# Kernel optimization log

Hardware: AMD Instinct MI355X
Metric: run time of the kernel (lower is better)

## Reference

```python
import jax, jax.numpy as jnp
import numpy as np

N_NODES = 50000
N_EDGES = 800000
N_GRAPHS = 100
IN_DIM = 100
OUT_DIM = 128
N_ETYPES = 4
N_STEPS = 8


def setup_inputs() -> dict:
    key = jax.random.key(0)
    ks = jax.random.split(key, 16)
    s = 0.05
    return {
        "features": jax.random.normal(ks[0], (N_NODES, IN_DIM), jnp.float32),
        "edge_src": jax.random.randint(ks[1], (N_EDGES,), 0, N_NODES, jnp.int32),
        "edge_dst": jax.random.randint(ks[2], (N_EDGES,), 0, N_NODES, jnp.int32),
        "edge_types": jax.random.randint(ks[3], (N_EDGES,), 0, N_ETYPES, jnp.int32),
        "graph_ids": jnp.sort(jax.random.randint(ks[4], (N_NODES,), 0, N_GRAPHS, jnp.int32)),
        "W_msg": jax.random.normal(ks[5], (N_ETYPES, OUT_DIM, OUT_DIM), jnp.float32) * s,
        "b_msg": jax.random.normal(ks[6], (N_ETYPES, OUT_DIM), jnp.float32) * s,
        "W_ih": jax.random.normal(ks[7], (3 * OUT_DIM, OUT_DIM), jnp.float32) * s,
        "W_hh": jax.random.normal(ks[8], (3 * OUT_DIM, OUT_DIM), jnp.float32) * s,
        "b_ih": jax.random.normal(ks[9], (3 * OUT_DIM,), jnp.float32) * s,
        "b_hh": jax.random.normal(ks[10], (3 * OUT_DIM,), jnp.float32) * s,
        "W1": jax.random.normal(ks[11], (256, OUT_DIM), jnp.float32) * s,
        "b1": jax.random.normal(ks[12], (256,), jnp.float32) * s,
        "W2": jax.random.normal(ks[13], (1, 256), jnp.float32) * s,
        "b2": jax.random.normal(ks[14], (1,), jnp.float32) * s,
    }


def _gru_cell(x, h, W_ih, W_hh, b_ih, b_hh):
    # torch.nn.GRUCell: gate order (reset, update, new)
    gi = x @ W_ih.T + b_ih  # [N, 3D]
    gh = h @ W_hh.T + b_hh
    i_r, i_z, i_n = jnp.split(gi, 3, axis=-1)
    h_r, h_z, h_n = jnp.split(gh, 3, axis=-1)
    r = jax.nn.sigmoid(i_r + h_r)
    z = jax.nn.sigmoid(i_z + h_z)
    n = jnp.tanh(i_n + r * h_n)
    return (1.0 - z) * n + z * h


def reference(features, edge_src, edge_dst, edge_types, graph_ids,
              W_msg, b_msg, W_ih, W_hh, b_ih, b_hh, W1, b1, W2, b2):
    n_nodes = features.shape[0]
    # DGL GatedGraphConv: zero-pad input features to out_feats
    h = jnp.pad(features, ((0, 0), (0, OUT_DIM - features.shape[1])))
    for _ in range(N_STEPS):
        # per-edge-type linear transform of source features: [T, N, D]
        transformed = jnp.einsum('nd,tdf->tnf', h, W_msg) + b_msg[:, None, :]
        msgs = transformed[edge_types, edge_src]  # [E, D] gather
        a = jax.ops.segment_sum(msgs, edge_dst, num_segments=n_nodes)  # scatter-add
        h = _gru_cell(a, h, W_ih, W_hh, b_ih, b_hh)
    # masked mean pooling per graph (mask_mean over de-batchified graphs)
    counts = jax.ops.segment_sum(jnp.ones((n_nodes,), h.dtype), graph_ids,
                                 num_segments=N_GRAPHS)
    sums = jax.ops.segment_sum(h, graph_ids, num_segments=N_GRAPHS)
    pooled = sums / jnp.maximum(counts, 1.0)[:, None]  # [B, D]
    # classifier: Linear -> relu -> (dropout: eval noop) -> Linear -> sigmoid
    hidden = jax.nn.relu(pooled @ W1.T + b1)
    logits = hidden @ W2.T + b2  # [B, 1]
    return jax.nn.sigmoid(logits).squeeze(-1)  # [B]
```

## Files before the change

kernel.cpp:

```cpp
#include <hip/hip_runtime.h>
#include <hip/hip_bf16.h>
#include <math.h>

#define N_NODES 50000
#define M_PAD   50048
#define N_EDGES 800000
#define N_GRAPHS 100
#define IN_DIM 100
#define D 128
#define N_STEPS 8
#define NBINS (N_NODES * 4)
#define SCAN_BLOCKS 196

typedef unsigned short ushort_t;
typedef __bf16 bf16x8 __attribute__((ext_vector_type(8)));
typedef float f32x4 __attribute__((ext_vector_type(4)));

__device__ inline ushort_t f2b(float f) {
  __hip_bfloat16 b = __float2bfloat16(f);
  return *reinterpret_cast<ushort_t*>(&b);
}
__device__ inline float b2f(unsigned int u16) {
  unsigned int x = u16 << 16;
  return __builtin_bit_cast(float, x);
}

__device__ __attribute__((always_inline)) inline void gld16(const ushort_t* g, ushort_t* l) {
  __builtin_amdgcn_global_load_lds(
      (const __attribute__((address_space(1))) void*)g,
      (__attribute__((address_space(3))) void*)l, 16, 0, 0);
}

__global__ void pad_cast_kernel(const float* __restrict__ feat, ushort_t* __restrict__ h) {
  int idx = blockIdx.x * blockDim.x + threadIdx.x;
  if (idx >= N_NODES * D) return;
  int n = idx >> 7, d = idx & 127;
  float v = (d < IN_DIM) ? feat[n * IN_DIM + d] : 0.0f;
  h[(size_t)n * 128 + d] = f2b(v);
}

__global__ void prep_bts(const float* __restrict__ W_msg, ushort_t* __restrict__ BtS) {
  int idx = blockIdx.x * blockDim.x + threadIdx.x;
  if (idx >= 128 * 512) return;
  int f = idx >> 9, kp = idx & 511;
  int t = kp >> 7, k = kp & 127;
  BtS[(size_t)f * 512 + kp] = f2b(W_msg[((size_t)t * 128 + k) * 128 + f]);
}

__global__ void prep_wg(const float* __restrict__ W_ih, const float* __restrict__ W_hh,
                        const float* __restrict__ b_ih, const float* __restrict__ b_hh,
                        ushort_t* __restrict__ WgT, float* __restrict__ gbias) {
  int idx = blockIdx.x * blockDim.x + threadIdx.x;
  if (idx >= 512 * 256) return;
  int colp = idx >> 8, k = idx & 255;
  int g = colp >> 6, gate = (colp >> 4) & 3, r = colp & 15;
  int d = g * 16 + r;
  float v;
  if (gate == 3)      v = (k < 128) ? 0.f : W_hh[(size_t)(256 + d) * 128 + (k - 128)];
  else if (gate == 2) v = (k < 128) ? W_ih[(size_t)(256 + d) * 128 + k] : 0.f;
  else {
    int j0 = (gate == 0) ? d : 128 + d;
    v = (k < 128) ? W_ih[(size_t)j0 * 128 + k] : W_hh[(size_t)j0 * 128 + (k - 128)];
  }
  WgT[(size_t)colp * 256 + k] = f2b(v);
  if (k == 0) {
    float bb = (gate == 0) ? b_ih[d] + b_hh[d]
             : (gate == 1) ? b_ih[128 + d] + b_hh[128 + d]
             : (gate == 2) ? b_ih[256 + d] : b_hh[256 + d];
    gbias[colp] = bb;
  }
}

__global__ void hist_kernel(const int* __restrict__ edst, const int* __restrict__ etype,
                            int* __restrict__ cnt2, int* __restrict__ rank) {
  int e = blockIdx.x * 256 + threadIdx.x;
  if (e >= N_EDGES) return;
  rank[e] = atomicAdd(&cnt2[edst[e] * 4 + etype[e]], 1);
}

__global__ __launch_bounds__(1024) void scanA(const int* __restrict__ cnt2,
                                              int* __restrict__ tmp, int* __restrict__ bsum) {
  __shared__ int wsum[16];
  int b = blockIdx.x, t = threadIdx.x;
  int i = b * 1024 + t;
  int lane = t & 63, wid = t >> 6;
  int x = (i < NBINS) ? cnt2[i] : 0;
  #pragma unroll
  for (int s = 1; s < 64; s <<= 1) {
    int y = __shfl_up(x, s, 64);
    if (lane >= s) x += y;
  }
  if (lane == 63) wsum[wid] = x;
  __syncthreads();
  if (wid == 0) {
    int w = (lane < 16) ? wsum[lane] : 0;
    #pragma unroll
    for (int s = 1; s < 16; s <<= 1) {
      int y = __shfl_up(w, s, 64);
      if (lane >= s) w += y;
    }
    if (lane < 16) wsum[lane] = w;
  }
  __syncthreads();
  int wb = (wid > 0) ? wsum[wid - 1] : 0;
  tmp[i] = wb + x;
  if (t == 1023) bsum[b] = wsum[15];
}

__global__ __launch_bounds__(64) void scanB(const int* __restrict__ bsum,
                                            int* __restrict__ bpre) {
  int lane = threadIdx.x;
  int carry = 0;
  for (int base = 0; base < SCAN_BLOCKS; base += 64) {
    int idx = base + lane;
    int v = (idx < SCAN_BLOCKS) ? bsum[idx] : 0;
    int x = v;
    #pragma unroll
    for (int s = 1; s < 64; s <<= 1) {
      int y = __shfl_up(x, s, 64);
      if (lane >= s) x += y;
    }
    if (idx < SCAN_BLOCKS) bpre[idx] = carry + x - v;
    carry += __shfl(x, 63, 64);
  }
}

__global__ __launch_bounds__(1024) void scanC(const int* __restrict__ tmp,
                                              const int* __restrict__ bpre,
                                              int* __restrict__ offs2) {
  int b = blockIdx.x, t = threadIdx.x;
  int i = b * 1024 + t;
  if (i < NBINS) offs2[i + 1] = tmp[i] + bpre[b];
  if (i == 0) offs2[0] = 0;
}

__global__ void fill_kernel(const int* __restrict__ esrc, const int* __restrict__ edst,
                            const int* __restrict__ etype, const int* __restrict__ offs2,
                            const int* __restrict__ rank, int* __restrict__ payload) {
  int e = blockIdx.x * 256 + threadIdx.x;
  if (e >= N_EDGES) return;
  int key = edst[e] * 4 + etype[e];
  payload[offs2[key] + rank[e]] = esrc[e];
}

__global__ __launch_bounds__(256) void gather_kernel(const int* __restrict__ offs2,
    const int* __restrict__ payload, const ushort_t* __restrict__ hb,
    ushort_t* __restrict__ S, float* __restrict__ cntf) {
  int n = blockIdx.x * 4 + (threadIdx.x >> 6);
  int lane = threadIdx.x & 63;
  if (n >= N_NODES) return;
  int bb[5];
  #pragma unroll
  for (int k = 0; k < 5; ++k) bb[k] = offs2[n * 4 + k];
  float a[4][2] = {{0.f, 0.f}, {0.f, 0.f}, {0.f, 0.f}, {0.f, 0.f}};
  const ushort_t* hrow = hb + lane * 2;
  for (int base = bb[0]; base < bb[4]; base += 64) {
    int lim = min(bb[4], base + 64);
    int cnt = lim - base;
    int pe = (lane < cnt) ? payload[base + lane] : 0;
    #pragma unroll
    for (int t = 0; t < 4; ++t) {
      int lo = max(bb[t], base), hi = min(bb[t + 1], lim);
      int i = lo;
      for (; i + 4 <= hi; i += 4) {
        int s0 = __shfl(pe, i - base, 64);
        int s1 = __shfl(pe, i + 1 - base, 64);
        int s2 = __shfl(pe, i + 2 - base, 64);
        int s3 = __shfl(pe, i + 3 - base, 64);
        unsigned int u0 = *(const unsigned int*)(hrow + (size_t)s0 * 128);
        unsigned int u1 = *(const unsigned int*)(hrow + (size_t)s1 * 128);
        unsigned int u2 = *(const unsigned int*)(hrow + (size_t)s2 * 128);
        unsigned int u3 = *(const unsigned int*)(hrow + (size_t)s3 * 128);
        a[t][0] += b2f(u0 & 0xffff) + b2f(u1 & 0xffff) + b2f(u2 & 0xffff) + b2f(u3 & 0xffff);
        a[t][1] += b2f(u0 >> 16) + b2f(u1 >> 16) + b2f(u2 >> 16) + b2f(u3 >> 16);
      }
      for (; i < hi; ++i) {
        int s0 = __shfl(pe, i - base, 64);
        unsigned int u0 = *(const unsigned int*)(hrow + (size_t)s0 * 128);
        a[t][0] += b2f(u0 & 0xffff);
        a[t][1] += b2f(u0 >> 16);
      }
    }
  }
  #pragma unroll
  for (int t = 0; t < 4; ++t) {
    unsigned int packed = (unsigned int)f2b(a[t][0]) | ((unsigned int)f2b(a[t][1]) << 16);
    *(unsigned int*)(S + (size_t)n * 512 + t * 128 + lane * 2) = packed;
    if (lane == 0) cntf[n * 4 + t] = (float)(bb[t + 1] - bb[t]);
  }
}

__global__ __launch_bounds__(512, 4) void mfma_msg(
    const ushort_t* __restrict__ S,
    const ushort_t* __restrict__ Bt,
    const float* __restrict__ b_msg, const float* __restrict__ cntf,
    ushort_t* __restrict__ a_out) {
  constexpr int K = 512;
  constexpr int NT  = K / 32;
  constexpr int PRE = 3;
  constexpr int SLOT = 16384;
  __shared__ __align__(16) unsigned char smem[SLOT * 4];
  const int m0 = blockIdx.x * 128;
  int tid = threadIdx.x;
  int wave = tid >> 6, lane = tid & 63;
  int wm = (wave & 3) * 32, wn = (wave >> 2) * 64;
  int quad = lane >> 4, l16 = lane & 15;

  int sr = lane >> 2, sc = lane & 3;
  const ushort_t* gA = S  + (size_t)(m0 + wave * 16 + sr) * K + sc * 8;
  const ushort_t* gB = Bt + (size_t)(wave * 16 + sr) * K + sc * 8;

  auto stage = [&](int slot, int t) {
    ushort_t* base = (ushort_t*)(smem + slot * SLOT);
    int k0 = t * 32;
    gld16(gA + k0, base + wave * 512);
    gld16(gB + k0, base + 4096 + wave * 512);
  };

  f32x4 acc[2][4];
  #pragma unroll
  for (int i = 0; i < 2; ++i)
    #pragma unroll
    for (int j = 0; j < 4; ++j) acc[i][j] = (f32x4){0.f, 0.f, 0.f, 0.f};

  #pragma unroll
  for (int t = 0; t < PRE; ++t) stage(t, t);

  #pragma unroll
  for (int t = 0; t < NT; ++t) {
    int infl = NT - 1 - t;
    if (infl >= 2)      asm volatile("s_waitcnt vmcnt(4) lgkmcnt(0)" ::: "memory");
    else if (infl == 1) asm volatile("s_waitcnt vmcnt(2) lgkmcnt(0)" ::: "memory");
    else                asm volatile("s_waitcnt vmcnt(0) lgkmcnt(0)" ::: "memory");
    __builtin_amdgcn_s_barrier();
    if (t + PRE < NT) stage((t + PRE) & 3, t + PRE);
    const ushort_t* As = (const ushort_t*)(smem + (t & 3) * SLOT);
    const ushort_t* Bs = As + 4096;
    bf16x8 af[2], bfr[4];
    #pragma unroll
    for (int i = 0; i < 2; ++i) af[i] = *(const bf16x8*)&As[(wm + i * 16 + l16) * 32 + quad * 8];
    #pragma unroll
    for (int j = 0; j < 4; ++j) bfr[j] = *(const bf16x8*)&Bs[(wn + j * 16 + l16) * 32 + quad * 8];
    #pragma unroll
    for (int i = 0; i < 2; ++i)
      #pragma unroll
      for (int j = 0; j < 4; ++j)
        acc[i][j] = __builtin_amdgcn_mfma_f32_16x16x32_bf16(af[i], bfr[j], acc[i][j], 0, 0, 0);
  }
  ushort_t* Ep = (ushort_t*)smem;
  float bm[4][4];
  #pragma unroll
  for (int j = 0; j < 4; ++j)
    #pragma unroll
    for (int t = 0; t < 4; ++t)
      bm[j][t] = b_msg[t * 128 + wn + j * 16 + l16];
  #pragma unroll
  for (int i = 0; i < 2; ++i)
    #pragma unroll
    for (int reg = 0; reg < 4; ++reg) {
      int row = wm + i * 16 + quad * 4 + reg;
      float4 c = *(const float4*)(cntf + (size_t)(m0 + row) * 4);
      #pragma unroll
      for (int j = 0; j < 4; ++j) {
        float val = acc[i][j][reg] + c.x * bm[j][0] + c.y * bm[j][1]
                                   + c.z * bm[j][2] + c.w * bm[j][3];
        Ep[row * 136 + wn + j * 16 + l16] = f2b(val);
      }
    }
  __syncthreads();
  #pragma unroll
  for (int c2 = 0; c2 < 4; ++c2) {
    int chunk = tid + 512 * c2;
    int row = chunk >> 4, sub = chunk & 15;
    *(uint4*)(a_out + (size_t)(m0 + row) * 128 + sub * 8) =
        *(const uint4*)&Ep[row * 136 + sub * 8];
  }
}

__global__ __launch_bounds__(512, 4) void mfma_gru(
    const ushort_t* __restrict__ Aa, const ushort_t* __restrict__ Ah,
    const ushort_t* __restrict__ Bt,
    const float* __restrict__ bias,
    ushort_t* __restrict__ h_out) {
  constexpr int K = 256;
  constexpr int NT  = K / 32;
  constexpr int PRE = 3;
  constexpr int SLOT = 16384;
  __shared__ __align__(16) unsigned char smem[SLOT * 4];
  int orig = blockIdx.x;
  int xcd = orig & 7, idxb = orig >> 3;
  int wgid = (xcd < 4 ? xcd * 196 : 4 * 196 + (xcd - 4) * 195) + idxb;
  const int m0 = (wgid >> 2) * 128, n0 = (wgid & 3) * 128;
  int tid = threadIdx.x;
  int wave = tid >> 6, lane = tid & 63;
  int wm = (wave & 3) * 32, wn = (wave >> 2) * 64;
  int quad = lane >> 4, l16 = lane & 15;

  int sr = lane >> 2, sc = lane & 3;
  const ushort_t* gAa = Aa + (size_t)(m0 + wave * 16 + sr) * 128 + sc * 8;
  const ushort_t* gAh = Ah + (size_t)(m0 + wave * 16 + sr) * 128 + sc * 8;
  const ushort_t* gB  = Bt + (size_t)(n0 + wave * 16 + sr) * K + sc * 8;

  auto stage = [&](int slot, int t) {
    ushort_t* base = (ushort_t*)(smem + slot * SLOT);
    const ushort_t* srcA = (t < 4) ? (gAa + t * 32) : (gAh + (t - 4) * 32);
    gld16(srcA, base + wave * 512);
    gld16(gB + t * 32, base + 4096 + wave * 512);
  };

  f32x4 acc[2][4];
  #pragma unroll
  for (int i = 0; i < 2; ++i)
    #pragma unroll
    for (int j = 0; j < 4; ++j) acc[i][j] = (f32x4){0.f, 0.f, 0.f, 0.f};

  #pragma unroll
  for (int t = 0; t < PRE; ++t) stage(t, t);

  #pragma unroll
  for (int t = 0; t < NT; ++t) {
    int infl = NT - 1 - t;
    if (infl >= 2)      asm volatile("s_waitcnt vmcnt(4) lgkmcnt(0)" ::: "memory");
    else if (infl == 1) asm volatile("s_waitcnt vmcnt(2) lgkmcnt(0)" ::: "memory");
    else                asm volatile("s_waitcnt vmcnt(0) lgkmcnt(0)" ::: "memory");
    __builtin_amdgcn_s_barrier();
    if (t + PRE < NT) stage((t + PRE) & 3, t + PRE);
    const ushort_t* As = (const ushort_t*)(smem + (t & 3) * SLOT);
    const ushort_t* Bs = As + 4096;
    bf16x8 af[2], bfr[4];
    #pragma unroll
    for (int i = 0; i < 2; ++i) af[i] = *(const bf16x8*)&As[(wm + i * 16 + l16) * 32 + quad * 8];
    #pragma unroll
    for (int j = 0; j < 4; ++j) bfr[j] = *(const bf16x8*)&Bs[(wn + j * 16 + l16) * 32 + quad * 8];
    #pragma unroll
    for (int i = 0; i < 2; ++i)
      #pragma unroll
      for (int j = 0; j < 4; ++j)
        acc[i][j] = __builtin_amdgcn_mfma_f32_16x16x32_bf16(af[i], bfr[j], acc[i][j], 0, 0, 0);
  }

  int wc = wave >> 2;
  const ushort_t* Hs = (const ushort_t*)(smem + (n0 >> 7) * SLOT);
  float hold_r[2][4];
  #pragma unroll
  for (int i = 0; i < 2; ++i)
    #pragma unroll
    for (int reg = 0; reg < 4; ++reg) {
      int r_loc = wm + i * 16 + quad * 4 + reg;
      hold_r[i][reg] = b2f(Hs[r_loc * 32 + wc * 16 + l16]);
    }
  asm volatile("s_waitcnt lgkmcnt(0)" ::: "memory");
  __builtin_amdgcn_s_barrier();

  ushort_t* Ap = (ushort_t*)smem;
  float br = bias[n0 + wn + l16];
  float bz = bias[n0 + wn + 16 + l16];
  float bi = bias[n0 + wn + 32 + l16];
  float bh = bias[n0 + wn + 48 + l16];
  #pragma unroll
  for (int i = 0; i < 2; ++i)
    #pragma unroll
    for (int reg = 0; reg < 4; ++reg) {
      int r_loc = wm + i * 16 + quad * 4 + reg;
      float pr  = acc[i][0][reg] + br;
      float pz  = acc[i][1][reg] + bz;
      float in_ = acc[i][2][reg] + bi;
      float hn  = acc[i][3][reg] + bh;
      float r = 1.0f / (1.0f + expf(-pr));
      float z = 1.0f / (1.0f + expf(-pz));
      float nn = tanhf(in_ + r * hn);
      float hv = (1.0f - z) * nn + z * hold_r[i][reg];
      Ap[r_loc * 40 + wc * 16 + l16] = f2b(hv);
    }
  __syncthreads();
  {
    int row = tid >> 2, sub = tid & 3;
    *(uint4*)(h_out + (size_t)(m0 + row) * 128 + (n0 >> 2) + sub * 8) =
        *(const uint4*)&Ap[row * 40 + sub * 8];
  }
}

__global__ __launch_bounds__(128) void pool_kernel(const ushort_t* __restrict__ h,
    const int* __restrict__ gids, float* __restrict__ pooled, float* __restrict__ gcnt) {
  __shared__ int lo_s, hi_s;
  int g = blockIdx.x, c = blockIdx.y, d = threadIdx.x;
  if (d == 0) {
    int lo = 0, hi = N_NODES;
    while (lo < hi) { int mid = (lo + hi) >> 1; if (gids[mid] < g) lo = mid + 1; else hi = mid; }
    lo_s = lo;
    int lo2 = lo, hi2 = N_NODES;
    while (lo2 < hi2) { int mid = (lo2 + hi2) >> 1; if (gids[mid] < g + 1) lo2 = mid + 1; else hi2 = mid; }
    hi_s = lo2;
  }
  __syncthreads();
  int lo = lo_s, hi = hi_s;
  int len = hi - lo;
  int b = lo + (int)(((long long)len * c) >> 3);
  int e = lo + (int)(((long long)len * (c + 1)) >> 3);
  float s = 0.f;
  for (int n = b; n < e; ++n) s += b2f(h[(size_t)n * 128 + d]);
  if (e > b) atomicAdd(&pooled[g * 128 + d], s);
  if (c == 0 && d == 0) gcnt[g] = (float)len;
}

__global__ __launch_bounds__(256) void classifier_kernel(
    const float* __restrict__ pooled, const float* __restrict__ gcnt,
    const float* __restrict__ W1, const float* __restrict__ b1,
    const float* __restrict__ W2, const float* __restrict__ b2,
    float* __restrict__ out) {
  __shared__ float p[D];
  __shared__ float hid[256];
  __shared__ float wsum[4];
  int g = blockIdx.x;
  int t = threadIdx.x;
  float cnt = fmaxf(gcnt[g], 1.0f);
  if (t < D) p[t] = pooled[g * D + t] / cnt;
  __syncthreads();
  float acc = b1[t];
  const float* w = W1 + (size_t)t * D;
  for (int k = 0; k < D; ++k) acc += p[k] * w[k];
  hid[t] = fmaxf(acc, 0.0f);
  __syncthreads();
  float v = hid[t] * W2[t];
  for (int off = 32; off > 0; off >>= 1) v += __shfl_down(v, off, 64);
  if ((t & 63) == 0) wsum[t >> 6] = v;
  __syncthreads();
  if (t == 0) {
    float s = wsum[0] + wsum[1] + wsum[2] + wsum[3] + b2[0];
    out[g] = 1.0f / (1.0f + expf(-s));
  }
}

extern "C" void kernel_launch(void* const* d_in, const int* in_sizes, int n_in,
                              void* d_out, int out_size, void* d_ws, size_t ws_size,
                              hipStream_t stream) {
  const float* features = (const float*)d_in[0];
  const int* esrc  = (const int*)d_in[1];
  const int* edst  = (const int*)d_in[2];
  const int* etype = (const int*)d_in[3];
  const int* gids  = (const int*)d_in[4];
  const float* W_msg = (const float*)d_in[5];
  const float* b_msg = (const float*)d_in[6];
  const float* W_ih  = (const float*)d_in[7];
  const float* W_hh  = (const float*)d_in[8];
  const float* b_ih  = (const float*)d_in[9];
  const float* b_hh  = (const float*)d_in[10];
  const float* W1 = (const float*)d_in[11];
  const float* b1 = (const float*)d_in[12];
  const float* W2 = (const float*)d_in[13];
  const float* b2 = (const float*)d_in[14];
  float* out = (float*)d_out;

  char* ws = (char*)d_ws;
  size_t off_b = 0;
  auto alloc = [&](size_t bytes) -> void* {
    void* p = ws + off_b;
    off_b += (bytes + 255) & ~(size_t)255;
    return p;
  };
  ushort_t* hA     = (ushort_t*)alloc((size_t)M_PAD * 128 * 2);
  ushort_t* hB     = (ushort_t*)alloc((size_t)M_PAD * 128 * 2);
  ushort_t* aArr   = (ushort_t*)alloc((size_t)M_PAD * 128 * 2);
  ushort_t* S      = (ushort_t*)alloc((size_t)M_PAD * 512 * 2);
  float*    cntf   = (float*)alloc((size_t)M_PAD * 4 * 4);
  ushort_t* BtS    = (ushort_t*)alloc(128 * 512 * 2);
  ushort_t* WgT    = (ushort_t*)alloc(512 * 256 * 2);
  float*    gbias  = (float*)alloc(512 * 4);
  int*      cnt2   = (int*)alloc((size_t)NBINS * 4);
  int*      offs2  = (int*)alloc((size_t)(NBINS + 1) * 4);
  int*      rank   = (int*)alloc((size_t)N_EDGES * 4);
  int*      tmp    = (int*)alloc((size_t)SCAN_BLOCKS * 1024 * 4);
  int*      bsum   = (int*)alloc(SCAN_BLOCKS * 4);
  int*      bpre   = (int*)alloc(SCAN_BLOCKS * 4);
  int*      payload= (int*)alloc((size_t)N_EDGES * 4);
  float*    pooled = (float*)alloc(N_GRAPHS * 128 * 4);
  float*    gcnt   = (float*)alloc(N_GRAPHS * 4);

  pad_cast_kernel<<<(N_NODES * 128 + 255) / 256, 256, 0, stream>>>(features, hA);
  prep_bts<<<(128 * 512 + 255) / 256, 256, 0, stream>>>(W_msg, BtS);
  prep_wg<<<(512 * 256 + 255) / 256, 256, 0, stream>>>(W_ih, W_hh, b_ih, b_hh, WgT, gbias);
  hipMemsetAsync(cnt2, 0, (size_t)NBINS * 4, stream);
  hist_kernel<<<(N_EDGES + 255) / 256, 256, 0, stream>>>(edst, etype, cnt2, rank);
  scanA<<<SCAN_BLOCKS, 1024, 0, stream>>>(cnt2, tmp, bsum);
  scanB<<<1, 64, 0, stream>>>(bsum, bpre);
  scanC<<<SCAN_BLOCKS, 1024, 0, stream>>>(tmp, bpre, offs2);
  fill_kernel<<<(N_EDGES + 255) / 256, 256, 0, stream>>>(esrc, edst, etype, offs2, rank, payload);

  ushort_t* hc = hA;
  ushort_t* hn = hB;
  for (int step = 0; step < N_STEPS; ++step) {
    gather_kernel<<<(N_NODES + 3) / 4, 256, 0, stream>>>(offs2, payload, hc, S, cntf);
    mfma_msg<<<M_PAD / 128, 512, 0, stream>>>(S, BtS, b_msg, cntf, aArr);
    mfma_gru<<<(M_PAD / 128) * 4, 512, 0, stream>>>(aArr, hc, WgT, gbias, hn);
    ushort_t* t2 = hc; hc = hn; hn = t2;
  }

  hipMemsetAsync(pooled, 0, (size_t)N_GRAPHS * 128 * 4, stream);
  pool_kernel<<<dim3(N_GRAPHS, 8), 128, 0, stream>>>(hc, gids, pooled, gcnt);
  classifier_kernel<<<N_GRAPHS, 256, 0, stream>>>(pooled, gcnt, W1, b1, W2, b2, out);
}
```

Measured before the change: 879.1 us.

## Remap msg GEMM blocks per XCD and shrink GRU pipeline to three stages

The message GEMM now remaps block IDs so each XCD processes a contiguous range of row tiles, which should improve L2 locality. The GRU GEMM drops from a four-slot, prefetch-depth-three LDS ring to a three-slot, depth-two ring, cutting shared memory per block so more blocks can be resident. It also reorders the K iterations so the h-tile this block needs for the epilogue is loaded last and is still in LDS afterwards. The cost is a shallower prefetch, which could expose more global-load latency.

```diff
diff --git a/kernel.cpp b/kernel.cpp
--- a/kernel.cpp
+++ b/kernel.cpp
@@ -200,7 +200,10 @@
   constexpr int PRE = 3;
   constexpr int SLOT = 16384;
   __shared__ __align__(16) unsigned char smem[SLOT * 4];
-  const int m0 = blockIdx.x * 128;
+  int orig = blockIdx.x;
+  int xcd = orig & 7, sidx = orig >> 3;
+  int wgb = (xcd < 7) ? (xcd * 49 + sidx) : (343 + sidx);
+  const int m0 = wgb * 128;
   int tid = threadIdx.x;
   int wave = tid >> 6, lane = tid & 63;
   int wm = (wave & 3) * 32, wn = (wave >> 2) * 64;
@@ -284,9 +287,8 @@
     ushort_t* __restrict__ h_out) {
   constexpr int K = 256;
   constexpr int NT  = K / 32;
-  constexpr int PRE = 3;
   constexpr int SLOT = 16384;
-  __shared__ __align__(16) unsigned char smem[SLOT * 4];
+  __shared__ __align__(16) unsigned char smem[SLOT * 3];
   int orig = blockIdx.x;
   int xcd = orig & 7, idxb = orig >> 3;
   int wgid = (xcd < 4 ? xcd * 196 : 4 * 196 + (xcd - 4) * 195) + idxb;
@@ -295,17 +297,26 @@
   int wave = tid >> 6, lane = tid & 63;
   int wm = (wave & 3) * 32, wn = (wave >> 2) * 64;
   int quad = lane >> 4, l16 = lane & 15;
+  const int q = n0 >> 7;
 
   int sr = lane >> 2, sc = lane & 3;
   const ushort_t* gAa = Aa + (size_t)(m0 + wave * 16 + sr) * 128 + sc * 8;
   const ushort_t* gAh = Ah + (size_t)(m0 + wave * 16 + sr) * 128 + sc * 8;
   const ushort_t* gB  = Bt + (size_t)(n0 + wave * 16 + sr) * K + sc * 8;
 
+  auto kglob = [&](int t) -> int {
+    if (t < 4) return t;
+    if (t == 7) return 4 + q;
+    int v = t - 4;
+    return 4 + v + (v >= q ? 1 : 0);
+  };
+
   auto stage = [&](int slot, int t) {
     ushort_t* base = (ushort_t*)(smem + slot * SLOT);
-    const ushort_t* srcA = (t < 4) ? (gAa + t * 32) : (gAh + (t - 4) * 32);
+    int kg = kglob(t);
+    const ushort_t* srcA = (kg < 4) ? (gAa + kg * 32) : (gAh + (kg - 4) * 32);
     gld16(srcA, base + wave * 512);
-    gld16(gB + t * 32, base + 4096 + wave * 512);
+    gld16(gB + kg * 32, base + 4096 + wave * 512);
   };
 
   f32x4 acc[2][4];
@@ -314,18 +325,16 @@
     #pragma unroll
     for (int j = 0; j < 4; ++j) acc[i][j] = (f32x4){0.f, 0.f, 0.f, 0.f};
 
-  #pragma unroll
-  for (int t = 0; t < PRE; ++t) stage(t, t);
+  stage(0, 0);
+  stage(1, 1);
 
   #pragma unroll
   for (int t = 0; t < NT; ++t) {
-    int infl = NT - 1 - t;
-    if (infl >= 2)      asm volatile("s_waitcnt vmcnt(4) lgkmcnt(0)" ::: "memory");
-    else if (infl == 1) asm volatile("s_waitcnt vmcnt(2) lgkmcnt(0)" ::: "memory");
-    else                asm volatile("s_waitcnt vmcnt(0) lgkmcnt(0)" ::: "memory");
+    if (t < NT - 1) asm volatile("s_waitcnt vmcnt(2) lgkmcnt(0)" ::: "memory");
+    else            asm volatile("s_waitcnt vmcnt(0) lgkmcnt(0)" ::: "memory");
     __builtin_amdgcn_s_barrier();
-    if (t + PRE < NT) stage((t + PRE) & 3, t + PRE);
-    const ushort_t* As = (const ushort_t*)(smem + (t & 3) * SLOT);
+    if (t + 2 < NT) stage((t + 2) % 3, t + 2);
+    const ushort_t* As = (const ushort_t*)(smem + (t % 3) * SLOT);
     const ushort_t* Bs = As + 4096;
     bf16x8 af[2], bfr[4];
     #pragma unroll
@@ -340,7 +349,7 @@
   }
 
   int wc = wave >> 2;
-  const ushort_t* Hs = (const ushort_t*)(smem + (n0 >> 7) * SLOT);
+  const ushort_t* Hs = (const ushort_t*)(smem + ((NT - 1) % 3) * SLOT);
   float hold_r[2][4];
   #pragma unroll
   for (int i = 0; i < 2; ++i)
```

Measured after the change: 866.5 us, median of 2. No clear change (-1.4%).
